# Performance work log

Hardware: AMD Instinct MI355X
Metric: run time of the kernel (lower is better)

## Reference

```python
import jax, jax.numpy as jnp
import numpy as np

N = 100000
E = 1000000
IN_C = 256
HID = 64
OUT = 64
NEG_SLOPE = 0.2


def setup_inputs() -> dict:
    key = jax.random.key(0)
    ks = jax.random.split(key, 12)
    x = jax.random.normal(ks[0], (N, IN_C), dtype=jnp.float32)
    edge_index = jax.random.randint(ks[1], (2, E), 0, N, dtype=jnp.int64)
    s = 1.0 / np.sqrt(IN_C)
    W1 = jax.random.uniform(ks[2], (IN_C, HID), jnp.float32, -s, s)
    a1_src = jax.random.uniform(ks[3], (HID,), jnp.float32, -s, s)
    a1_dst = jax.random.uniform(ks[4], (HID,), jnp.float32, -s, s)
    b1 = jnp.zeros((HID,), jnp.float32)
    s2 = 1.0 / np.sqrt(HID)
    W2 = jax.random.uniform(ks[5], (HID, OUT), jnp.float32, -s2, s2)
    a2_src = jax.random.uniform(ks[6], (OUT,), jnp.float32, -s2, s2)
    a2_dst = jax.random.uniform(ks[7], (OUT,), jnp.float32, -s2, s2)
    b2 = jnp.zeros((OUT,), jnp.float32)
    return {"x": x, "edge_index": edge_index, "W1": W1, "a1_src": a1_src,
            "a1_dst": a1_dst, "b1": b1, "W2": W2, "a2_src": a2_src,
            "a2_dst": a2_dst, "b2": b2}


def gat_conv(x, W, a_src, a_dst, b, src, dst):
    h = x @ W                              # [N, d]
    alpha_s = h @ a_src                    # [N]
    alpha_d = h @ a_dst                    # [N]
    e = jax.nn.leaky_relu(alpha_s[src] + alpha_d[dst], NEG_SLOPE)  # [E]
    # segment softmax over incoming edges of each destination node
    e_max = jax.lax.stop_gradient(jax.ops.segment_max(e, dst, num_segments=N))
    ex = jnp.exp(e - e_max[dst])
    denom = jax.ops.segment_sum(ex, dst, num_segments=N)
    alpha = ex / (denom[dst] + 1e-16)      # [E]
    out = jax.ops.segment_sum(alpha[:, None] * h[src], dst, num_segments=N)
    return out + b


def reference(x, edge_index, W1, a1_src, a1_dst, b1, W2, a2_src, a2_dst, b2):
    src, dst = edge_index[0], edge_index[1]
    # dropout(p=0.6) is identity in eval mode
    h = jax.nn.relu(gat_conv(x, W1, a1_src, a1_dst, b1, src, dst))
    out = gat_conv(h, W2, a2_src, a2_dst, b2, src, dst)
    return out
```

## Files before the change

### kernel.cpp

```cpp
#include <hip/hip_runtime.h>
#include <math.h>

#define HID 64
#define BSH 9
#define NPB 512
#define EPB 4096
#define CAP 8192

typedef __attribute__((ext_vector_type(8))) short bf16x8;
typedef __attribute__((ext_vector_type(4))) float f32x4;
typedef __attribute__((ext_vector_type(4))) unsigned int u32x4;

__device__ __forceinline__ unsigned short f2bf(float f) {
    unsigned u = __float_as_uint(f);
    unsigned r = u + 0x7FFF + ((u >> 16) & 1);
    return (unsigned short)(r >> 16);
}
__device__ __forceinline__ float bf2f(unsigned short b) {
    return __uint_as_float(((unsigned)b) << 16);
}


__global__ __launch_bounds__(256) void prep_kernel(const float* __restrict__ W1,
                                                   const float* __restrict__ W2,
                                                   unsigned short* __restrict__ Wt1,
                                                   unsigned short* __restrict__ Wt2,
                                                   int* __restrict__ bcnt) {
    int t = threadIdx.x, blk = blockIdx.x;
    int n = t & 63;
    if (blk == 0) bcnt[t] = 0;
    if (blk < 64) {
        int k = blk * 4 + (t >> 6);
        Wt1[(size_t)n * 256 + k] = f2bf(W1[(size_t)k * 64 + n]);
    } else {
        int k = (blk - 64) * 4 + (t >> 6);
        Wt2[(size_t)n * 64 + k] = f2bf(W2[(size_t)k * 64 + n]);
    }
}


__global__ __launch_bounds__(256) void bucket_scatter(const int* __restrict__ esrc,
                                                      const int* __restrict__ edst,
                                                      int* __restrict__ bcnt,
                                                      int* __restrict__ ebuf, int E_, int NB) {
    __shared__ int hist[256], chunk[256], lcur[256];
    int t = threadIdx.x;
    hist[t] = 0;
    lcur[t] = 0;
    __syncthreads();
    int base = blockIdx.x * EPB;
    int s[EPB / 256], d[EPB / 256];
#pragma unroll
    for (int r = 0; r < EPB / 256; ++r) {
        int i = base + r * 256 + t;
        if (i < E_) {
            s[r] = esrc[i];
            d[r] = edst[i];
            atomicAdd(&hist[d[r] >> BSH], 1);
        } else {
            d[r] = -1;
        }
    }
    __syncthreads();
    if (t < NB) chunk[t] = hist[t] ? atomicAdd(&bcnt[t], hist[t]) : 0;
    __syncthreads();
#pragma unroll
    for (int r = 0; r < EPB / 256; ++r) {
        if (d[r] >= 0) {
            int b = d[r] >> BSH;
            int pos = chunk[b] + atomicAdd(&lcur[b], 1);
            ebuf[b * CAP + pos] = (s[r] << BSH) | (d[r] & (NPB - 1));
        }
    }
}

__global__ __launch_bounds__(256) void csr_build(const int* __restrict__ ebuf,
                                                 const int* __restrict__ bcnt,
                                                 int2* __restrict__ offs,
                                                 int* __restrict__ srcs, int Nv) {
    __shared__ int dhist[NPB], dbase[NPB], psum[256];
    int b = blockIdx.x, t = threadIdx.x;
    int cnt = bcnt[b];
    int e0 = b * CAP;
#pragma unroll
    for (int j = t; j < NPB; j += 256) dhist[j] = 0;
    __syncthreads();
    for (int i = t; i < cnt; i += 256) {
        atomicAdd(&dhist[ebuf[e0 + i] & (NPB - 1)], 1);
    }
    __syncthreads();
    int a0 = dhist[2 * t], a1 = dhist[2 * t + 1];
    psum[t] = a0 + a1;
    __syncthreads();
    for (int o = 1; o < 256; o <<= 1) {
        int u = (t >= o) ? psum[t - o] : 0;
        __syncthreads();
        psum[t] += u;
        __syncthreads();
    }
    int ex = psum[t] - (a0 + a1);
    dbase[2 * t] = ex;
    dbase[2 * t + 1] = ex + a0;
    __syncthreads();
#pragma unroll
    for (int j = t; j < NPB; j += 256) {
        int node = (b << BSH) + j;
        if (node < Nv) {
            int beg = e0 + dbase[j];
            offs[node] = make_int2(beg, beg + dhist[j]);
        }
    }
    __syncthreads();
    for (int i = t; i < cnt; i += 256) {
        int e = ebuf[e0 + i];
        int pos = atomicAdd(&dbase[e & (NPB - 1)], 1);
        srcs[e0 + pos] = e >> BSH;
    }
}


template <int K, bool BF16IN>
__global__ __launch_bounds__(256) void gemm_mfma(const void* __restrict__ Xv,
                                                 const unsigned short* __restrict__ Wt,
                                                 const float* __restrict__ a_s,
                                                 const float* __restrict__ a_d,
                                                 unsigned short* __restrict__ C,
                                                 float* __restrict__ as_,
                                                 float* __restrict__ ad_, int Nrows) {
    constexpr int KPAD = K + 8;
    constexpr int XPAD = 72;
    __shared__ __align__(16) unsigned short Ws[64 * KPAD];
    __shared__ __align__(16) unsigned short Xs[128 * XPAD];

    const float* Xf = (const float*)Xv;
    const unsigned short* Xb = (const unsigned short*)Xv;

    int t = threadIdx.x;
    int n0 = blockIdx.x * 128;
    int lane = t & 63;
    int w = t >> 6;
    int m = lane & 15;
    int q = lane >> 4;
    int base = n0 + w * 32;

    constexpr int KC8 = K / 8;
    for (int i = t; i < 64 * KC8; i += 256) {
        int n = i / KC8;
        int kc = i % KC8;
        u32x4 v = *(const u32x4*)(Wt + (size_t)n * K + kc * 8);
        *(u32x4*)(&Ws[n * KPAD + kc * 8]) = v;
    }

    f32x4 acc[2][4];
#pragma unroll
    for (int mi = 0; mi < 2; ++mi)
#pragma unroll
        for (int ct = 0; ct < 4; ++ct) acc[mi][ct] = (f32x4){0.f, 0.f, 0.f, 0.f};

    for (int k0 = 0; k0 < K; k0 += 64) {
        if (!BF16IN) {
#pragma unroll
            for (int i = 0; i < 8; ++i) {
                int idx = i * 256 + t;
                int row = idx >> 4;
                int kq = (idx & 15) * 4;
                int gn = n0 + row;
                if (gn >= Nrows) gn = Nrows - 1;
                float4 v = *(const float4*)(Xf + (size_t)gn * K + k0 + kq);
                ushort4 bb;
                bb.x = f2bf(v.x); bb.y = f2bf(v.y); bb.z = f2bf(v.z); bb.w = f2bf(v.w);
                *(ushort4*)(&Xs[row * XPAD + kq]) = bb;
            }
        } else {
#pragma unroll
            for (int i = 0; i < 4; ++i) {
                int idx = i * 256 + t;
                int row = idx >> 3;
                int kq = (idx & 7) * 8;
                int gn = n0 + row;
                if (gn >= Nrows) gn = Nrows - 1;
                u32x4 v = *(const u32x4*)(Xb + (size_t)gn * K + k0 + kq);
                *(u32x4*)(&Xs[row * XPAD + kq]) = v;
            }
        }
        __syncthreads();
#pragma unroll
        for (int ks = 0; ks < 64; ks += 32) {
            bf16x8 a0 = *(const bf16x8*)(&Xs[(w * 32 + m) * XPAD + ks + q * 8]);
            bf16x8 a1 = *(const bf16x8*)(&Xs[(w * 32 + 16 + m) * XPAD + ks + q * 8]);
#pragma unroll
            for (int ct = 0; ct < 4; ++ct) {
                bf16x8 bv = *(const bf16x8*)(&Ws[(ct * 16 + m) * KPAD + k0 + ks + q * 8]);
                acc[0][ct] = __builtin_amdgcn_mfma_f32_16x16x32_bf16(a0, bv, acc[0][ct], 0, 0, 0);
                acc[1][ct] = __builtin_amdgcn_mfma_f32_16x16x32_bf16(a1, bv, acc[1][ct], 0, 0, 0);
            }
        }
        __syncthreads();
    }

    float sa0 = a_s[m], sa1 = a_s[16 + m], sa2 = a_s[32 + m], sa3 = a_s[48 + m];
    float da0 = a_d[m], da1 = a_d[16 + m], da2 = a_d[32 + m], da3 = a_d[48 + m];

#pragma unroll
    for (int mi = 0; mi < 2; ++mi) {
#pragma unroll
        for (int r = 0; r < 4; ++r) {
            int row = base + mi * 16 + q * 4 + r;
            if (row < Nrows) {
                size_t ro = (size_t)row * 64 + m;
                C[ro]      = f2bf(acc[mi][0][r]);
                C[ro + 16] = f2bf(acc[mi][1][r]);
                C[ro + 32] = f2bf(acc[mi][2][r]);
                C[ro + 48] = f2bf(acc[mi][3][r]);
            }
        }
        float vs[4], vd[4];
#pragma unroll
        for (int r = 0; r < 4; ++r) {
            float s = acc[mi][0][r] * sa0 + acc[mi][1][r] * sa1 +
                      acc[mi][2][r] * sa2 + acc[mi][3][r] * sa3;
            float d = acc[mi][0][r] * da0 + acc[mi][1][r] * da1 +
                      acc[mi][2][r] * da2 + acc[mi][3][r] * da3;
#pragma unroll
            for (int o = 1; o < 16; o <<= 1) {
                s += __shfl_xor(s, o);
                d += __shfl_xor(d, o);
            }
            vs[r] = s;
            vd[r] = d;
        }
        if (m < 4) {
            int row = base + mi * 16 + q * 4 + m;
            float wvs = (m == 0) ? vs[0] : (m == 1) ? vs[1] : (m == 2) ? vs[2] : vs[3];
            float wvd = (m == 0) ? vd[0] : (m == 1) ? vd[1] : (m == 2) ? vd[2] : vd[3];
            if (row < Nrows) {
                as_[row] = wvs;
                ad_[row] = wvd;
            }
        }
    }
}


template <bool RELU_BF16OUT>
__global__ __launch_bounds__(256) void agg_kernel(const unsigned short* __restrict__ H,
                                                  const float* __restrict__ as_,
                                                  const float* __restrict__ ad_,
                                                  const float* __restrict__ bias,
                                                  const int2* __restrict__ offs,
                                                  const int* __restrict__ srcs,
                                                  void* __restrict__ outp, int Nrows) {
    int t = threadIdx.x;
    int lane = t & 63;
    int l32 = lane & 31;
    int hsel = lane & 32;
    int d = blockIdx.x * 8 + ((t >> 6) << 1) + (hsel >> 5);
    if (d >= Nrows) return;
    int2 oe = offs[d];
    int begin = oe.x;
    int cnt = oe.y - oe.x;
    if (cnt > 64) cnt = 64;
    float adv = ad_[d];

    int sa = 0, sb = 0;
    float pa = 0.f, pb = 0.f;
    if (l32 < cnt) {
        sa = srcs[begin + l32];
        float xv = as_[sa] + adv;
        xv = (xv > 0.f) ? xv : 0.2f * xv;
        pa = __expf(xv);
    }
    if (32 + l32 < cnt) {
        sb = srcs[begin + 32 + l32];
        float xv = as_[sb] + adv;
        xv = (xv > 0.f) ? xv : 0.2f * xv;
        pb = __expf(xv);
    }
    float lsum = pa + pb;
#pragma unroll
    for (int o = 1; o < 32; o <<= 1) lsum += __shfl_xor(lsum, o);

    float acc0 = 0.f, acc1 = 0.f;
    const unsigned short* Hp = H + 2 * l32;
    int nbA = (cnt < 32 ? cnt : 32);
    nbA = (nbA + 7) & ~7;
    for (int j = 0; j < nbA; j += 8) {
        unsigned hv[8];
        float pv[8];
#pragma unroll
        for (int u = 0; u < 8; ++u) {
            int idx = hsel | (j + u);
            int su = __shfl(sa, idx);
            pv[u] = __shfl(pa, idx);
            hv[u] = *(const unsigned*)(Hp + (size_t)su * HID);
        }
#pragma unroll
        for (int u = 0; u < 8; ++u) {
            acc0 += pv[u] * __uint_as_float(hv[u] << 16);
            acc1 += pv[u] * __uint_as_float(hv[u] & 0xFFFF0000u);
        }
    }
    int cb = cnt - 32;
    if (cb > 0) {
        int nbB = (cb + 7) & ~7;
        for (int j = 0; j < nbB; j += 8) {
            unsigned hv[8];
            float pv[8];
#pragma unroll
            for (int u = 0; u < 8; ++u) {
                int idx = hsel | (j + u);
                int su = __shfl(sb, idx);
                pv[u] = __shfl(pb, idx);
                hv[u] = *(const unsigned*)(Hp + (size_t)su * HID);
            }
#pragma unroll
            for (int u = 0; u < 8; ++u) {
                acc0 += pv[u] * __uint_as_float(hv[u] << 16);
                acc1 += pv[u] * __uint_as_float(hv[u] & 0xFFFF0000u);
            }
        }
    }

    float inv = 1.f / (lsum + 1e-16f);
    float2 bv = *(const float2*)(bias + 2 * l32);
    float o0 = acc0 * inv + bv.x;
    float o1 = acc1 * inv + bv.y;
    if (RELU_BF16OUT) {
        unsigned pkd = ((unsigned)f2bf(fmaxf(o1, 0.f)) << 16) | f2bf(fmaxf(o0, 0.f));
        *(unsigned*)((unsigned short*)outp + (size_t)d * HID + 2 * l32) = pkd;
    } else {
        *(float2*)((float*)outp + (size_t)d * HID + 2 * l32) = make_float2(o0, o1);
    }
}


extern "C" void kernel_launch(void* const* d_in, const int* in_sizes, int n_in,
                              void* d_out, int out_size, void* d_ws, size_t ws_size,
                              hipStream_t stream) {
    const float* x      = (const float*)d_in[0];
    const int*   edge   = (const int*)d_in[1];
    const float* W1     = (const float*)d_in[2];
    const float* a1_src = (const float*)d_in[3];
    const float* a1_dst = (const float*)d_in[4];
    const float* b1     = (const float*)d_in[5];
    const float* W2     = (const float*)d_in[6];
    const float* a2_src = (const float*)d_in[7];
    const float* a2_dst = (const float*)d_in[8];
    const float* b2     = (const float*)d_in[9];
    float* out = (float*)d_out;

    const int N = in_sizes[0] / 256;
    const int E = in_sizes[1] / 2;
    const int IN_C = 256;
    const int NB = (N + NPB - 1) >> BSH;

    char* w = (char*)d_ws;
    auto alloc = [&](size_t bytes) {
        char* p = w;
        w += (bytes + 255) & ~(size_t)255;
        return p;
    };
    int2*           offs = (int2*)alloc((size_t)N * 8);
    int*            srcs = (int*)alloc((size_t)NB * CAP * 4);
    int*            ebuf = (int*)alloc((size_t)NB * CAP * 4);
    int*            bcnt = (int*)alloc(256 * 4);
    unsigned short* h1   = (unsigned short*)alloc((size_t)N * HID * 2);
    unsigned short* hB   = (unsigned short*)alloc((size_t)N * HID * 2);
    float*          as_  = (float*)alloc((size_t)N * 4);
    float*          ad_  = (float*)alloc((size_t)N * 4);
    unsigned short* Wt1  = (unsigned short*)alloc((size_t)IN_C * 64 * 2);
    unsigned short* Wt2  = (unsigned short*)alloc((size_t)64 * 64 * 2);

    const int* esrc = edge;
    const int* edst = edge + E;

    prep_kernel<<<IN_C / 4 + 64 / 4, 256, 0, stream>>>(W1, W2, Wt1, Wt2, bcnt);

    int gbk = (E + EPB - 1) / EPB;
    bucket_scatter<<<gbk, 256, 0, stream>>>(esrc, edst, bcnt, ebuf, E, NB);
    csr_build<<<NB, 256, 0, stream>>>(ebuf, bcnt, offs, srcs, N);

    int gblocks = (N + 127) / 128;
    int ablocks = (N + 7) / 8;

    gemm_mfma<256, false><<<gblocks, 256, 0, stream>>>(x, Wt1, a1_src, a1_dst, h1, as_, ad_, N);
    agg_kernel<true><<<ablocks, 256, 0, stream>>>(h1, as_, ad_, b1, offs, srcs, hB, N);

    gemm_mfma<64, true><<<gblocks, 256, 0, stream>>>(hB, Wt2, a2_src, a2_dst, h1, as_, ad_, N);
    agg_kernel<false><<<ablocks, 256, 0, stream>>>(h1, as_, ad_, b2, offs, srcs, out, N);
}
```

Baseline: 285.5 us.

## Fuse edge bucket scatter with layer-1 GEMM and widen aggregation lanes

Merges the edge bucketing kernel and the first MFMA GEMM into one launch, with the first blocks doing the scatter and the rest computing the projection, so the two independent phases can overlap on the GPU. The scatter now rereads the edge arrays from global memory instead of keeping them in registers. Aggregation now uses 16 lanes per destination node with 8-byte gathers of four features each, up from 32 lanes with two features, so each block handles 16 nodes. This aims to cut launch overhead and make the gathers wider, at the cost of a larger shared-memory union and more work per lane.

```diff
diff --git a/kernel.cpp b/kernel.cpp
--- a/kernel.cpp
+++ b/kernel.cpp
@@ -10,14 +10,12 @@
 typedef __attribute__((ext_vector_type(8))) short bf16x8;
 typedef __attribute__((ext_vector_type(4))) float f32x4;
 typedef __attribute__((ext_vector_type(4))) unsigned int u32x4;
+typedef __attribute__((ext_vector_type(2))) unsigned int u32x2;
 
 __device__ __forceinline__ unsigned short f2bf(float f) {
     unsigned u = __float_as_uint(f);
     unsigned r = u + 0x7FFF + ((u >> 16) & 1);
     return (unsigned short)(r >> 16);
-}
-__device__ __forceinline__ float bf2f(unsigned short b) {
-    return __uint_as_float(((unsigned)b) << 16);
 }
 
 
@@ -39,40 +37,137 @@
 }
 
 
-__global__ __launch_bounds__(256) void bucket_scatter(const int* __restrict__ esrc,
-                                                      const int* __restrict__ edst,
-                                                      int* __restrict__ bcnt,
-                                                      int* __restrict__ ebuf, int E_, int NB) {
-    __shared__ int hist[256], chunk[256], lcur[256];
+__global__ __launch_bounds__(256) void scatter_gemm1(
+    const int* __restrict__ esrc, const int* __restrict__ edst,
+    int* __restrict__ bcnt, int* __restrict__ ebuf, int E_, int NB, int SB,
+    const float* __restrict__ Xf, const unsigned short* __restrict__ Wt,
+    const float* __restrict__ a_s, const float* __restrict__ a_d,
+    unsigned short* __restrict__ C, float* __restrict__ as_,
+    float* __restrict__ ad_, int Nrows) {
+    constexpr int K = 256, KPAD = K + 8, XPAD = 72;
+    __shared__ union {
+        unsigned short gemm[64 * KPAD + 128 * XPAD];
+        struct { int hist[256]; int chunk[256]; int lcur[256]; } sc;
+    } sh;
     int t = threadIdx.x;
-    hist[t] = 0;
-    lcur[t] = 0;
-    __syncthreads();
-    int base = blockIdx.x * EPB;
-    int s[EPB / 256], d[EPB / 256];
-#pragma unroll
-    for (int r = 0; r < EPB / 256; ++r) {
-        int i = base + r * 256 + t;
-        if (i < E_) {
-            s[r] = esrc[i];
-            d[r] = edst[i];
-            atomicAdd(&hist[d[r] >> BSH], 1);
-        } else {
-            d[r] = -1;
-        }
-    }
-    __syncthreads();
-    if (t < NB) chunk[t] = hist[t] ? atomicAdd(&bcnt[t], hist[t]) : 0;
-    __syncthreads();
-#pragma unroll
-    for (int r = 0; r < EPB / 256; ++r) {
-        if (d[r] >= 0) {
-            int b = d[r] >> BSH;
-            int pos = chunk[b] + atomicAdd(&lcur[b], 1);
-            ebuf[b * CAP + pos] = (s[r] << BSH) | (d[r] & (NPB - 1));
-        }
-    }
-}
+
+    if ((int)blockIdx.x < SB) {
+        sh.sc.hist[t] = 0;
+        sh.sc.lcur[t] = 0;
+        __syncthreads();
+        int base = blockIdx.x * EPB;
+        int lim = E_ - base;
+        if (lim > EPB) lim = EPB;
+        for (int i = t; i < lim; i += 256) {
+            atomicAdd(&sh.sc.hist[edst[base + i] >> BSH], 1);
+        }
+        __syncthreads();
+        if (t < NB) sh.sc.chunk[t] = sh.sc.hist[t] ? atomicAdd(&bcnt[t], sh.sc.hist[t]) : 0;
+        __syncthreads();
+        for (int i = t; i < lim; i += 256) {
+            int sv = esrc[base + i];
+            int dv = edst[base + i];
+            int b = dv >> BSH;
+            int pos = sh.sc.chunk[b] + atomicAdd(&sh.sc.lcur[b], 1);
+            ebuf[b * CAP + pos] = (sv << BSH) | (dv & (NPB - 1));
+        }
+        return;
+    }
+
+    unsigned short* Ws = sh.gemm;
+    unsigned short* Xs = sh.gemm + 64 * KPAD;
+    int n0 = ((int)blockIdx.x - SB) * 128;
+    int lane = t & 63;
+    int w = t >> 6;
+    int m = lane & 15;
+    int q = lane >> 4;
+    int base = n0 + w * 32;
+
+    constexpr int KC8 = K / 8;
+    for (int i = t; i < 64 * KC8; i += 256) {
+        int n = i / KC8;
+        int kc = i % KC8;
+        u32x4 v = *(const u32x4*)(Wt + (size_t)n * K + kc * 8);
+        *(u32x4*)(&Ws[n * KPAD + kc * 8]) = v;
+    }
+
+    f32x4 acc[2][4];
+#pragma unroll
+    for (int mi = 0; mi < 2; ++mi)
+#pragma unroll
+        for (int ct = 0; ct < 4; ++ct) acc[mi][ct] = (f32x4){0.f, 0.f, 0.f, 0.f};
+
+    for (int k0 = 0; k0 < K; k0 += 64) {
+#pragma unroll
+        for (int i = 0; i < 8; ++i) {
+            int idx = i * 256 + t;
+            int row = idx >> 4;
+            int kq = (idx & 15) * 4;
+            int gn = n0 + row;
+            if (gn >= Nrows) gn = Nrows - 1;
+            float4 v = *(const float4*)(Xf + (size_t)gn * K + k0 + kq);
+            ushort4 bb;
+            bb.x = f2bf(v.x); bb.y = f2bf(v.y); bb.z = f2bf(v.z); bb.w = f2bf(v.w);
+            *(ushort4*)(&Xs[row * XPAD + kq]) = bb;
+        }
+        __syncthreads();
+#pragma unroll
+        for (int ks = 0; ks < 64; ks += 32) {
+            bf16x8 a0 = *(const bf16x8*)(&Xs[(w * 32 + m) * XPAD + ks + q * 8]);
+            bf16x8 a1 = *(const bf16x8*)(&Xs[(w * 32 + 16 + m) * XPAD + ks + q * 8]);
+#pragma unroll
+            for (int ct = 0; ct < 4; ++ct) {
+                bf16x8 bv = *(const bf16x8*)(&Ws[(ct * 16 + m) * KPAD + k0 + ks + q * 8]);
+                acc[0][ct] = __builtin_amdgcn_mfma_f32_16x16x32_bf16(a0, bv, acc[0][ct], 0, 0, 0);
+                acc[1][ct] = __builtin_amdgcn_mfma_f32_16x16x32_bf16(a1, bv, acc[1][ct], 0, 0, 0);
+            }
+        }
+        __syncthreads();
+    }
+
+    float sa0 = a_s[m], sa1 = a_s[16 + m], sa2 = a_s[32 + m], sa3 = a_s[48 + m];
+    float da0 = a_d[m], da1 = a_d[16 + m], da2 = a_d[32 + m], da3 = a_d[48 + m];
+
+#pragma unroll
+    for (int mi = 0; mi < 2; ++mi) {
+#pragma unroll
+        for (int r = 0; r < 4; ++r) {
+            int row = base + mi * 16 + q * 4 + r;
+            if (row < Nrows) {
+                size_t ro = (size_t)row * 64 + m;
+                C[ro]      = f2bf(acc[mi][0][r]);
+                C[ro + 16] = f2bf(acc[mi][1][r]);
+                C[ro + 32] = f2bf(acc[mi][2][r]);
+                C[ro + 48] = f2bf(acc[mi][3][r]);
+            }
+        }
+        float vs[4], vd[4];
+#pragma unroll
+        for (int r = 0; r < 4; ++r) {
+            float s = acc[mi][0][r] * sa0 + acc[mi][1][r] * sa1 +
+                      acc[mi][2][r] * sa2 + acc[mi][3][r] * sa3;
+            float d = acc[mi][0][r] * da0 + acc[mi][1][r] * da1 +
+                      acc[mi][2][r] * da2 + acc[mi][3][r] * da3;
+#pragma unroll
+            for (int o = 1; o < 16; o <<= 1) {
+                s += __shfl_xor(s, o);
+                d += __shfl_xor(d, o);
+            }
+            vs[r] = s;
+            vd[r] = d;
+        }
+        if (m < 4) {
+            int row = base + mi * 16 + q * 4 + m;
+            float wvs = (m == 0) ? vs[0] : (m == 1) ? vs[1] : (m == 2) ? vs[2] : vs[3];
+            float wvd = (m == 0) ? vd[0] : (m == 1) ? vd[1] : (m == 2) ? vd[2] : vd[3];
+            if (row < Nrows) {
+                as_[row] = wvs;
+                ad_[row] = wvd;
+            }
+        }
+    }
+}
+
 
 __global__ __launch_bounds__(256) void csr_build(const int* __restrict__ ebuf,
                                                  const int* __restrict__ bcnt,
@@ -242,6 +337,30 @@
 }
 
 
+#define GATHER_CHUNK(sC, pC, BASE_E)                                          \
+    {                                                                         \
+        int rem = cnt - (BASE_E);                                             \
+        if (rem > 0) {                                                        \
+            int nb = rem < 16 ? ((rem + 7) & ~7) : 16;                        \
+            for (int j = 0; j < nb; j += 8) {                                 \
+                u32x2 hv[8];                                                  \
+                float pv[8];                                                  \
+                _Pragma("unroll") for (int u = 0; u < 8; ++u) {               \
+                    int idx = qsel | (j + u);                                 \
+                    int su = __shfl(sC, idx);                                 \
+                    pv[u] = __shfl(pC, idx);                                  \
+                    hv[u] = *(const u32x2*)(Hp + (size_t)su * HID);           \
+                }                                                             \
+                _Pragma("unroll") for (int u = 0; u < 8; ++u) {               \
+                    acc0 += pv[u] * __uint_as_float(hv[u].x << 16);           \
+                    acc1 += pv[u] * __uint_as_float(hv[u].x & 0xFFFF0000u);   \
+                    acc2 += pv[u] * __uint_as_float(hv[u].y << 16);           \
+                    acc3 += pv[u] * __uint_as_float(hv[u].y & 0xFFFF0000u);   \
+                }                                                             \
+            }                                                                 \
+        }                                                                     \
+    }
+
 template <bool RELU_BF16OUT>
 __global__ __launch_bounds__(256) void agg_kernel(const unsigned short* __restrict__ H,
                                                   const float* __restrict__ as_,
@@ -252,9 +371,9 @@
                                                   void* __restrict__ outp, int Nrows) {
     int t = threadIdx.x;
     int lane = t & 63;
-    int l32 = lane & 31;
-    int hsel = lane & 32;
-    int d = blockIdx.x * 8 + ((t >> 6) << 1) + (hsel >> 5);
+    int q16 = lane & 15;
+    int qsel = lane & 48;
+    int d = blockIdx.x * 16 + ((t >> 6) << 2) + (qsel >> 4);
     if (d >= Nrows) return;
     int2 oe = offs[d];
     int begin = oe.x;
@@ -262,74 +381,57 @@
     if (cnt > 64) cnt = 64;
     float adv = ad_[d];
 
-    int sa = 0, sb = 0;
-    float pa = 0.f, pb = 0.f;
-    if (l32 < cnt) {
-        sa = srcs[begin + l32];
-        float xv = as_[sa] + adv;
+    int s0 = 0, s1 = 0, s2 = 0, s3 = 0;
+    float p0 = 0.f, p1 = 0.f, p2 = 0.f, p3 = 0.f;
+    if (q16 < cnt) {
+        s0 = srcs[begin + q16];
+        float xv = as_[s0] + adv;
         xv = (xv > 0.f) ? xv : 0.2f * xv;
-        pa = __expf(xv);
-    }
-    if (32 + l32 < cnt) {
-        sb = srcs[begin + 32 + l32];
-        float xv = as_[sb] + adv;
+        p0 = __expf(xv);
+    }
+    if (16 + q16 < cnt) {
+        s1 = srcs[begin + 16 + q16];
+        float xv = as_[s1] + adv;
         xv = (xv > 0.f) ? xv : 0.2f * xv;
-        pb = __expf(xv);
-    }
-    float lsum = pa + pb;
-#pragma unroll
-    for (int o = 1; o < 32; o <<= 1) lsum += __shfl_xor(lsum, o);
-
-    float acc0 = 0.f, acc1 = 0.f;
-    const unsigned short* Hp = H + 2 * l32;
-    int nbA = (cnt < 32 ? cnt : 32);
-    nbA = (nbA + 7) & ~7;
-    for (int j = 0; j < nbA; j += 8) {
-        unsigned hv[8];
-        float pv[8];
-#pragma unroll
-        for (int u = 0; u < 8; ++u) {
-            int idx = hsel | (j + u);
-            int su = __shfl(sa, idx);
-            pv[u] = __shfl(pa, idx);
-            hv[u] = *(const unsigned*)(Hp + (size_t)su * HID);
-        }
-#pragma unroll
-        for (int u = 0; u < 8; ++u) {
-            acc0 += pv[u] * __uint_as_float(hv[u] << 16);
-            acc1 += pv[u] * __uint_as_float(hv[u] & 0xFFFF0000u);
-        }
-    }
-    int cb = cnt - 32;
-    if (cb > 0) {
-        int nbB = (cb + 7) & ~7;
-        for (int j = 0; j < nbB; j += 8) {
-            unsigned hv[8];
-            float pv[8];
-#pragma unroll
-            for (int u = 0; u < 8; ++u) {
-                int idx = hsel | (j + u);
-                int su = __shfl(sb, idx);
-                pv[u] = __shfl(pb, idx);
-                hv[u] = *(const unsigned*)(Hp + (size_t)su * HID);
-            }
-#pragma unroll
-            for (int u = 0; u < 8; ++u) {
-                acc0 += pv[u] * __uint_as_float(hv[u] << 16);
-                acc1 += pv[u] * __uint_as_float(hv[u] & 0xFFFF0000u);
-            }
-        }
-    }
+        p1 = __expf(xv);
+    }
+    if (32 + q16 < cnt) {
+        s2 = srcs[begin + 32 + q16];
+        float xv = as_[s2] + adv;
+        xv = (xv > 0.f) ? xv : 0.2f * xv;
+        p2 = __expf(xv);
+    }
+    if (48 + q16 < cnt) {
+        s3 = srcs[begin + 48 + q16];
+        float xv = as_[s3] + adv;
+        xv = (xv > 0.f) ? xv : 0.2f * xv;
+        p3 = __expf(xv);
+    }
+    float lsum = (p0 + p1) + (p2 + p3);
+#pragma unroll
+    for (int o = 1; o < 16; o <<= 1) lsum += __shfl_xor(lsum, o);
+
+    float acc0 = 0.f, acc1 = 0.f, acc2 = 0.f, acc3 = 0.f;
+    const unsigned short* Hp = H + 4 * q16;
+    GATHER_CHUNK(s0, p0, 0)
+    GATHER_CHUNK(s1, p1, 16)
+    GATHER_CHUNK(s2, p2, 32)
+    GATHER_CHUNK(s3, p3, 48)
 
     float inv = 1.f / (lsum + 1e-16f);
-    float2 bv = *(const float2*)(bias + 2 * l32);
+    float4 bv = *(const float4*)(bias + 4 * q16);
     float o0 = acc0 * inv + bv.x;
     float o1 = acc1 * inv + bv.y;
+    float o2 = acc2 * inv + bv.z;
+    float o3 = acc3 * inv + bv.w;
     if (RELU_BF16OUT) {
-        unsigned pkd = ((unsigned)f2bf(fmaxf(o1, 0.f)) << 16) | f2bf(fmaxf(o0, 0.f));
-        *(unsigned*)((unsigned short*)outp + (size_t)d * HID + 2 * l32) = pkd;
+        u32x2 pkd;
+        pkd.x = ((unsigned)f2bf(fmaxf(o1, 0.f)) << 16) | f2bf(fmaxf(o0, 0.f));
+        pkd.y = ((unsigned)f2bf(fmaxf(o3, 0.f)) << 16) | f2bf(fmaxf(o2, 0.f));
+        *(u32x2*)((unsigned short*)outp + (size_t)d * HID + 4 * q16) = pkd;
     } else {
-        *(float2*)((float*)outp + (size_t)d * HID + 2 * l32) = make_float2(o0, o1);
+        *(float4*)((float*)outp + (size_t)d * HID + 4 * q16) =
+            make_float4(o0, o1, o2, o3);
     }
 }
 
@@ -376,14 +478,13 @@
 
     prep_kernel<<<IN_C / 4 + 64 / 4, 256, 0, stream>>>(W1, W2, Wt1, Wt2, bcnt);
 
-    int gbk = (E + EPB - 1) / EPB;
-    bucket_scatter<<<gbk, 256, 0, stream>>>(esrc, edst, bcnt, ebuf, E, NB);
+    int SB = (E + EPB - 1) / EPB;
+    int gblocks = (N + 127) / 128;
+    scatter_gemm1<<<SB + gblocks, 256, 0, stream>>>(esrc, edst, bcnt, ebuf, E, NB, SB,
+                                                    x, Wt1, a1_src, a1_dst, h1, as_, ad_, N);
     csr_build<<<NB, 256, 0, stream>>>(ebuf, bcnt, offs, srcs, N);
 
-    int gblocks = (N + 127) / 128;
-    int ablocks = (N + 7) / 8;
-
-    gemm_mfma<256, false><<<gblocks, 256, 0, stream>>>(x, Wt1, a1_src, a1_dst, h1, as_, ad_, N);
+    int ablocks = (N + 15) / 16;
     agg_kernel<true><<<ablocks, 256, 0, stream>>>(h1, as_, ad_, b1, offs, srcs, hB, N);
 
     gemm_mfma<64, true><<<gblocks, 256, 0, stream>>>(hB, Wt2, a2_src, a2_dst, h1, as_, ad_, N);
```

After: 269.2 us. -5.7%, faster.
